# Optimization experiments

Hardware: AMD Instinct MI355X
Metric: run time of the kernel (lower is better)

Reference implementation:

```python
import jax, jax.numpy as jnp
import numpy as np
import math

N_HEAD = 16

def _rope(x):
    # x: [B, H, T, D], D even; interleaved-pair rotation as in the torch code
    B, H, T, D = x.shape
    theta = 10000.0 ** (-2.0 * jnp.arange(D // 2, dtype=x.dtype) / D)  # [D/2]
    pos = jnp.arange(T, dtype=x.dtype)[:, None]                        # [T,1]
    ang = pos * theta[None, :]                                          # [T, D/2]
    sin, cos = jnp.sin(ang), jnp.cos(ang)
    x1, x2 = x[..., ::2], x[..., 1::2]
    x1r = x1 * cos - x2 * sin
    x2r = x1 * sin + x2 * cos
    # re-interleave
    out = jnp.stack([x1r, x2r], axis=-1).reshape(B, H, T, D)
    return out

def setup_inputs() -> dict:
    key = jax.random.key(0)
    ks = jax.random.split(key, 3)
    B, T, C = 4, 2048, 1024
    x = jax.random.normal(ks[0], (B, T, C), dtype=jnp.float32)
    W_qkv = jax.random.normal(ks[1], (C, 3 * C), dtype=jnp.float32) * (1.0 / math.sqrt(C))
    b_qkv = jnp.zeros((3 * C,), dtype=jnp.float32)
    W_proj = jax.random.normal(ks[2], (C, C), dtype=jnp.float32) * (1.0 / math.sqrt(C))
    b_proj = jnp.zeros((C,), dtype=jnp.float32)
    return {"x": x, "W_qkv": W_qkv, "b_qkv": b_qkv, "W_proj": W_proj, "b_proj": b_proj}

def reference(x, W_qkv, b_qkv, W_proj, b_proj):
    B, T, C = x.shape
    H = N_HEAD
    D = C // H
    qkv = x @ W_qkv + b_qkv                      # [B,T,3C]
    q, k, v = jnp.split(qkv, 3, axis=-1)
    def to_heads(t):
        return t.reshape(B, T, H, D).transpose(0, 2, 1, 3)  # [B,H,T,D]
    q, k, v = to_heads(q), to_heads(k), to_heads(v)
    q = _rope(q)
    k = _rope(k)
    att = jnp.einsum('bhqd,bhkd->bhqk', q, k) * (1.0 / math.sqrt(D))
    mask = jnp.tril(jnp.ones((T, T), dtype=bool))
    att = jnp.where(mask[None, None, :, :], att, -jnp.inf)
    att = jax.nn.softmax(att, axis=-1)
    y = jnp.einsum('bhqk,bhkd->bhqd', att, v)    # [B,H,T,D]
    y = y.transpose(0, 2, 1, 3).reshape(B, T, C)
    return y @ W_proj + b_proj
```

## Files before the change

kernel.cpp:

```cpp
#include <hip/hip_runtime.h>
#include <cstddef>

#define B_DIM 4
#define T_DIM 2048
#define C_DIM 1024
#define H_DIM 16
#define D_DIM 64
#define C3_DIM 3072

typedef __attribute__((ext_vector_type(8))) _Float16 f16x8;
typedef __attribute__((ext_vector_type(4))) _Float16 f16x4;
typedef __attribute__((ext_vector_type(4))) float f32x4;

typedef const __attribute__((address_space(1))) unsigned int* gptr_t;
typedef __attribute__((address_space(3))) unsigned int* lptr_t;

#define QSCALE 0.180336850073f
#define NTHETA 0.41524101186f

__global__ __launch_bounds__(256) void prep(
    const float* __restrict__ x, _Float16* __restrict__ xh,
    const float* __restrict__ Wq, _Float16* __restrict__ Wqt,
    const float* __restrict__ Wp, _Float16* __restrict__ Wpt)
{
    __shared__ float tile[64][65];
    const int z = blockIdx.x, tid = threadIdx.x;

    if (z < 8192) {
        size_t i = (size_t)z * 1024 + tid * 4;
        float4 v = *(const float4*)&x[i];
        f16x4 o = { (_Float16)v.x, (_Float16)v.y, (_Float16)v.z, (_Float16)v.w };
        *(f16x4*)&xh[i] = o;
        return;
    }

    const float* W;
    _Float16* Wt;
    int N, idx;
    if (z < 8960) { W = Wq; Wt = Wqt; N = C3_DIM; idx = z - 8192; }
    else          { W = Wp; Wt = Wpt; N = C_DIM;  idx = z - 8960; }
    const int K = C_DIM;
    const int nblk = N / 64;
    const int n0 = (idx % nblk) * 64, k0 = (idx / nblk) * 64;

    const int tx = tid & 15, ty = tid >> 4;
#pragma unroll
    for (int it = 0; it < 4; ++it) {
        int r = it * 16 + ty;
        *(float4*)&tile[r][tx * 4] =
            *(const float4*)&W[(size_t)(k0 + r) * N + n0 + tx * 4];
    }
    __syncthreads();
    int c = tid >> 2, t0 = (tid & 3) * 16;
    __align__(16) _Float16 tmp[16];
#pragma unroll
    for (int j = 0; j < 16; ++j) tmp[j] = (_Float16)tile[t0 + j][c];
    _Float16* o = Wt + (size_t)(n0 + c) * K + k0 + t0;
    *(f16x8*)o = *(f16x8*)&tmp[0];
    *(f16x8*)(o + 8) = *(f16x8*)&tmp[8];
}

#define ISSUE_SLICE(BUF, S, KT)                                               \
    do {                                                                      \
        const _Float16* agk = ag + (KT) * 64 + (S) * 32;                      \
        const _Float16* bgk = bg + (KT) * 64 + (S) * 32;                      \
        __builtin_amdgcn_global_load_lds((gptr_t)(const void*)(agk),          \
            (lptr_t)(void*)&Af[BUF][S][w * 2 + 0][0][0], 16, 0, 0);           \
        __builtin_amdgcn_global_load_lds((gptr_t)(const void*)(agk + 16 * K), \
            (lptr_t)(void*)&Af[BUF][S][w * 2 + 1][0][0], 16, 0, 0);           \
        __builtin_amdgcn_global_load_lds((gptr_t)(const void*)(bgk),          \
            (lptr_t)(void*)&Bf[BUF][S][w][0][0], 16, 0, 0);                   \
    } while (0)

#define COMPUTE_SLICE(BUF, S, SWAPPED)                                        \
    do {                                                                      \
        f16x8 av[4], bv[4];                                                   \
        _Pragma("unroll")                                                     \
        for (int i = 0; i < 4; ++i) {                                         \
            av[i] = *(const f16x8*)&Af[BUF][S][wm * 4 + i][lane][0];          \
            bv[i] = *(const f16x8*)&Bf[BUF][S][wn * 4 + i][lane][0];          \
        }                                                                     \
        __builtin_amdgcn_s_setprio(1);                                        \
        _Pragma("unroll")                                                     \
        for (int i = 0; i < 4; ++i)                                           \
            _Pragma("unroll")                                                 \
            for (int j = 0; j < 4; ++j)                                       \
                acc[i][j] = (SWAPPED)                                         \
                    ? __builtin_amdgcn_mfma_f32_16x16x32_f16(                 \
                          bv[j], av[i], acc[i][j], 0, 0, 0)                   \
                    : __builtin_amdgcn_mfma_f32_16x16x32_f16(                 \
                          av[i], bv[j], acc[i][j], 0, 0, 0);                  \
        __builtin_amdgcn_s_setprio(0);                                        \
    } while (0)

#define KLOOP(SWAPPED)                                                        \
    do {                                                                      \
        const int NT = K / 64;                                                \
        ISSUE_SLICE(0, 0, 0);                                                 \
        ISSUE_SLICE(0, 1, 0);                                                 \
        for (int t = 0; t < NT - 1; ++t) {                                    \
            const int cb = t & 1, nb = cb ^ 1;                                \
            ISSUE_SLICE(nb, 0, t + 1);                                        \
            asm volatile("s_waitcnt vmcnt(6)" ::: "memory");                  \
            __builtin_amdgcn_s_barrier();                                     \
            COMPUTE_SLICE(cb, 0, SWAPPED);                                    \
            ISSUE_SLICE(nb, 1, t + 1);                                        \
            asm volatile("s_waitcnt vmcnt(6)" ::: "memory");                  \
            __builtin_amdgcn_s_barrier();                                     \
            COMPUTE_SLICE(cb, 1, SWAPPED);                                    \
        }                                                                     \
        {                                                                     \
            const int cb = (NT - 1) & 1;                                      \
            asm volatile("s_waitcnt vmcnt(3)" ::: "memory");                  \
            __builtin_amdgcn_s_barrier();                                     \
            COMPUTE_SLICE(cb, 0, SWAPPED);                                    \
            asm volatile("s_waitcnt vmcnt(0)" ::: "memory");                  \
            __builtin_amdgcn_s_barrier();                                     \
            COMPUTE_SLICE(cb, 1, SWAPPED);                                    \
        }                                                                     \
    } while (0)

__global__ __launch_bounds__(512, 2) void gemm_qkv(
    const _Float16* __restrict__ A, const _Float16* __restrict__ Bt,
    const float* __restrict__ bias,
    _Float16* __restrict__ Qb, _Float16* __restrict__ Kb, _Float16* __restrict__ Vt)
{
    __shared__ __align__(16) _Float16 Af[2][2][16][64][8];
    __shared__ __align__(16) _Float16 Bf[2][2][8][64][8];
    const int tid = threadIdx.x;
    const int lane = tid & 63, w = tid >> 6;
    const int lm = lane & 15, lq = lane >> 4;
    const int wm = w >> 1, wn = w & 1;
    const int m0 = blockIdx.y * 256, n0 = blockIdx.x * 128;
    const int K = C_DIM;

    const _Float16* ag = A + (size_t)(m0 + w * 32 + lm) * K + lq * 8;
    const _Float16* bg = Bt + (size_t)(n0 + w * 16 + lm) * K + lq * 8;

    f32x4 acc[4][4];
#pragma unroll
    for (int i = 0; i < 4; ++i)
#pragma unroll
        for (int j = 0; j < 4; ++j) acc[i][j] = (f32x4){0.f, 0.f, 0.f, 0.f};

    const bool is_v = (n0 >= 2 * C_DIM);

    if (!is_v) {
        KLOOP(true);

        const bool is_q = (n0 < C_DIM);
        const float scale = is_q ? QSCALE : 1.0f;
        _Float16* dstbase = is_q ? Qb : Kb;
#pragma unroll
        for (int j = 0; j < 4; ++j) {
            int col = n0 + wn * 64 + j * 16 + lq * 4;
            int d0 = col & 63;
            int h = (col & (C_DIM - 1)) >> 6;
            float4 b4 = *(const float4*)&bias[col];
            float th0 = exp2f(-NTHETA * (float)(d0 >> 1));
            float th1 = exp2f(-NTHETA * (float)((d0 >> 1) + 1));
#pragma unroll
            for (int i = 0; i < 4; ++i) {
                int tg = m0 + wm * 64 + i * 16 + lm;
                int bb = tg >> 11, tl = tg & (T_DIM - 1);
                float v0 = acc[i][j][0] + b4.x;
                float v1 = acc[i][j][1] + b4.y;
                float v2 = acc[i][j][2] + b4.z;
                float v3 = acc[i][j][3] + b4.w;
                float s0, c0, s1, c1;
                __sincosf((float)tl * th0, &s0, &c0);
                __sincosf((float)tl * th1, &s1, &c1);
                f16x4 o = { (_Float16)((v0 * c0 - v1 * s0) * scale),
                            (_Float16)((v0 * s0 + v1 * c0) * scale),
                            (_Float16)((v2 * c1 - v3 * s1) * scale),
                            (_Float16)((v2 * s1 + v3 * c1) * scale) };
                *(f16x4*)&dstbase[((size_t)(bb * 16 + h) * T_DIM + tl) * 64 + d0] = o;
            }
        }
    } else {
        KLOOP(false);

#pragma unroll
        for (int i = 0; i < 4; ++i) {
            int t4 = m0 + wm * 64 + i * 16 + lq * 4;
            int bb = t4 >> 11, tl = t4 & (T_DIM - 1);
#pragma unroll
            for (int j = 0; j < 4; ++j) {
                int col = n0 + wn * 64 + j * 16 + lm;
                int dfull = col - 2 * C_DIM;
                int h = dfull >> 6, d = dfull & 63;
                float bc = bias[col];
                f16x4 o = { (_Float16)(acc[i][j][0] + bc),
                            (_Float16)(acc[i][j][1] + bc),
                            (_Float16)(acc[i][j][2] + bc),
                            (_Float16)(acc[i][j][3] + bc) };
                *(f16x4*)&Vt[((size_t)(bb * 16 + h) * 64 + d) * T_DIM + tl] = o;
            }
        }
    }
}

template <bool OUT_HALF>
__global__ __launch_bounds__(512, 2) void gemm_bt(
    const _Float16* __restrict__ A, const _Float16* __restrict__ Bt,
    const float* __restrict__ bias, void* __restrict__ Cout,
    int M, int N, int K)
{
    __shared__ __align__(16) _Float16 Af[2][2][16][64][8];
    __shared__ __align__(16) _Float16 Bf[2][2][8][64][8];
    const int tid = threadIdx.x;
    const int lane = tid & 63, w = tid >> 6;
    const int lm = lane & 15, lq = lane >> 4;
    const int wm = w >> 1, wn = w & 1;
    const int m0 = blockIdx.y * 256, n0 = blockIdx.x * 128;

    const _Float16* ag = A + (size_t)(m0 + w * 32 + lm) * K + lq * 8;
    const _Float16* bg = Bt + (size_t)(n0 + w * 16 + lm) * K + lq * 8;

    f32x4 acc[4][4];
#pragma unroll
    for (int i = 0; i < 4; ++i)
#pragma unroll
        for (int j = 0; j < 4; ++j) acc[i][j] = (f32x4){0.f, 0.f, 0.f, 0.f};

    KLOOP(true);

#pragma unroll
    for (int i = 0; i < 4; ++i) {
        size_t row = (size_t)(m0 + wm * 64 + i * 16 + lm);
#pragma unroll
        for (int j = 0; j < 4; ++j) {
            int col = n0 + wn * 64 + j * 16 + lq * 4;
            float4 b4 = *(const float4*)&bias[col];
            float v0 = acc[i][j][0] + b4.x;
            float v1 = acc[i][j][1] + b4.y;
            float v2 = acc[i][j][2] + b4.z;
            float v3 = acc[i][j][3] + b4.w;
            if (OUT_HALF) {
                f16x4 o = { (_Float16)v0, (_Float16)v1, (_Float16)v2, (_Float16)v3 };
                *(f16x4*)&((_Float16*)Cout)[row * N + col] = o;
            } else {
                float4 o = make_float4(v0, v1, v2, v3);
                *(float4*)&((float*)Cout)[row * N + col] = o;
            }
        }
    }
}

__global__ __launch_bounds__(256) void attn_mfma(
    const _Float16* __restrict__ Qb, const _Float16* __restrict__ Kb,
    const _Float16* __restrict__ Vt, _Float16* __restrict__ yb)
{
    __shared__ __align__(16) _Float16 Kf[8][64][8];
    __shared__ __align__(16) _Float16 Vf[8][64][8];
    __shared__ __align__(16) _Float16 Pb[4][16][88];

    const int tid = threadIdx.x;
    const int bh = blockIdx.x;
    const int qt = 31 - blockIdx.y;
    const int b = bh >> 4, h = bh & 15;
    const int lane = tid & 63, w = tid >> 6;
    const int m = lane & 15, qq = lane >> 4;

    const _Float16* qrow = Qb +
        ((size_t)bh * T_DIM + qt * 64 + w * 16 + m) * D_DIM + qq * 8;
    f16x8 qreg[2];
    qreg[0] = *(const f16x8*)qrow;
    qreg[1] = *(const f16x8*)(qrow + 32);

    float l_i = 0.f;
    f32x4 acc[4];
#pragma unroll
    for (int db = 0; db < 4; ++db) acc[db] = (f32x4){0.f, 0.f, 0.f, 0.f};

    const _Float16* kg0 = Kb + (size_t)bh * T_DIM * D_DIM +
                          (size_t)(w * 16 + m) * D_DIM + qq * 8;
    const _Float16* vg0 = Vt + (size_t)bh * D_DIM * T_DIM +
                          (size_t)(w * 16 + m) * T_DIM + qq * 8;

    f16x8 kr0 = *(const f16x8*)(kg0);
    f16x8 kr1 = *(const f16x8*)(kg0 + 32);
    f16x8 vr0 = *(const f16x8*)(vg0);
    f16x8 vr1 = *(const f16x8*)(vg0 + 32);

    for (int kt = 0; kt <= qt; ++kt) {
        __syncthreads();
        *(f16x8*)&Kf[w * 2 + 0][lane][0] = kr0;
        *(f16x8*)&Kf[w * 2 + 1][lane][0] = kr1;
        *(f16x8*)&Vf[w * 2 + 0][lane][0] = vr0;
        *(f16x8*)&Vf[w * 2 + 1][lane][0] = vr1;
        __syncthreads();

        int ktn = (kt < qt) ? kt + 1 : kt;
        kr0 = *(const f16x8*)(kg0 + (size_t)ktn * 64 * D_DIM);
        kr1 = *(const f16x8*)(kg0 + (size_t)ktn * 64 * D_DIM + 32);
        vr0 = *(const f16x8*)(vg0 + ktn * 64);
        vr1 = *(const f16x8*)(vg0 + ktn * 64 + 32);

        f32x4 sv[4];
#pragma unroll
        for (int nb = 0; nb < 4; ++nb) {
            f32x4 s = (f32x4){0.f, 0.f, 0.f, 0.f};
            s = __builtin_amdgcn_mfma_f32_16x16x32_f16(
                *(const f16x8*)&Kf[nb * 2 + 0][lane][0], qreg[0], s, 0, 0, 0);
            s = __builtin_amdgcn_mfma_f32_16x16x32_f16(
                *(const f16x8*)&Kf[nb * 2 + 1][lane][0], qreg[1], s, 0, 0, 0);
            sv[nb] = s;
        }

        if (kt == qt) {
            int qlocal = w * 16 + m;
#pragma unroll
            for (int nb = 0; nb < 4; ++nb) {
                int tb = nb * 16 + qq * 4;
#pragma unroll
                for (int r = 0; r < 4; ++r)
                    if (tb + r > qlocal) sv[nb][r] = -1e30f;
            }
        }

        float ll = 0.f;
#pragma unroll
        for (int nb = 0; nb < 4; ++nb) {
            float p0 = exp2f(sv[nb][0]);
            float p1 = exp2f(sv[nb][1]);
            float p2 = exp2f(sv[nb][2]);
            float p3 = exp2f(sv[nb][3]);
            sv[nb][0] = p0; sv[nb][1] = p1; sv[nb][2] = p2; sv[nb][3] = p3;
            ll += (p0 + p1) + (p2 + p3);
        }
        l_i += ll;

#pragma unroll
        for (int nb = 0; nb < 4; ++nb) {
            f16x4 pv = { (_Float16)sv[nb][0], (_Float16)sv[nb][1],
                         (_Float16)sv[nb][2], (_Float16)sv[nb][3] };
            *(f16x4*)&Pb[w][m][nb * 16 + qq * 4] = pv;
        }

        f16x8 pf0 = *(const f16x8*)&Pb[w][m][0 * 32 + qq * 8];
        f16x8 pf1 = *(const f16x8*)&Pb[w][m][1 * 32 + qq * 8];

#pragma unroll
        for (int db = 0; db < 4; ++db) {
            acc[db] = __builtin_amdgcn_mfma_f32_16x16x32_f16(
                *(const f16x8*)&Vf[db * 2 + 0][lane][0], pf0, acc[db], 0, 0, 0);
            acc[db] = __builtin_amdgcn_mfma_f32_16x16x32_f16(
                *(const f16x8*)&Vf[db * 2 + 1][lane][0], pf1, acc[db], 0, 0, 0);
        }
    }

    l_i += __shfl_xor(l_i, 16);
    l_i += __shfl_xor(l_i, 32);

    float inv = 1.0f / l_i;
    _Float16* yrow = yb + (size_t)(b * T_DIM + qt * 64 + w * 16 + m) * C_DIM +
                     h * D_DIM + qq * 4;
#pragma unroll
    for (int db = 0; db < 4; ++db) {
        f16x4 o = { (_Float16)(acc[db][0] * inv), (_Float16)(acc[db][1] * inv),
                    (_Float16)(acc[db][2] * inv), (_Float16)(acc[db][3] * inv) };
        *(f16x4*)(yrow + db * 16) = o;
    }
}

extern "C" void kernel_launch(void* const* d_in, const int* in_sizes, int n_in,
                              void* d_out, int out_size, void* d_ws, size_t ws_size,
                              hipStream_t stream)
{
    const float* x     = (const float*)d_in[0];
    const float* Wqkv  = (const float*)d_in[1];
    const float* bqkv  = (const float*)d_in[2];
    const float* Wproj = (const float*)d_in[3];
    const float* bproj = (const float*)d_in[4];
    float* out = (float*)d_out;

    char* ws = (char*)d_ws;
    _Float16* xh  = (_Float16*)(ws);
    _Float16* yh  = (_Float16*)(ws + 16777216ull);
    _Float16* Qb  = (_Float16*)(ws + 33554432ull);
    _Float16* Kb  = (_Float16*)(ws + 50331648ull);
    _Float16* Vt  = (_Float16*)(ws + 67108864ull);
    _Float16* Wqt = (_Float16*)(ws + 83886080ull);
    _Float16* Wpt = (_Float16*)(ws + 90177536ull);

    prep<<<dim3(9216), dim3(256), 0, stream>>>(x, xh, Wqkv, Wqt, Wproj, Wpt);

    gemm_qkv<<<dim3(C3_DIM / 128, (B_DIM * T_DIM) / 256), dim3(512), 0, stream>>>(
        xh, Wqt, bqkv, Qb, Kb, Vt);

    attn_mfma<<<dim3(B_DIM * H_DIM, T_DIM / 64), dim3(256), 0, stream>>>(
        Qb, Kb, Vt, yh);

    gemm_bt<false><<<dim3(C_DIM / 128, (B_DIM * T_DIM) / 256), dim3(512), 0, stream>>>(
        yh, Wpt, bproj, out, B_DIM * T_DIM, C_DIM, C_DIM);
}
```

Before: 287.0 us.

## Double-buffer attention K/V tiles with direct global-to-LDS async loads

Replaces the register-staged K/V prefetch in the attention kernel with global_load_lds transfers into a double-buffered LDS tile. The next tile's loads are issued before computing on the current one, synchronised with vmcnt waits and raw s_barrier. This removes VGPR staging and the LDS store step, and aims to overlap memory latency with MFMA work. In exchange it doubles K/V LDS use, and correctness relies on hand-written waitcnt values and the LDS address layout that the direct-to-LDS builtin writes.

```diff
diff --git a/kernel.cpp b/kernel.cpp
--- a/kernel.cpp
+++ b/kernel.cpp
@@ -247,12 +247,26 @@
     }
 }
 
+#define ATTN_ISSUE_KV(BUF, KT)                                                \
+    do {                                                                      \
+        const _Float16* kgk = kg0 + (size_t)(KT) * 64 * D_DIM;                \
+        const _Float16* vgk = vg0 + (KT) * 64;                                \
+        __builtin_amdgcn_global_load_lds((gptr_t)(const void*)(kgk),          \
+            (lptr_t)(void*)&Kf[BUF][w * 2 + 0][0][0], 16, 0, 0);              \
+        __builtin_amdgcn_global_load_lds((gptr_t)(const void*)(kgk + 32),     \
+            (lptr_t)(void*)&Kf[BUF][w * 2 + 1][0][0], 16, 0, 0);              \
+        __builtin_amdgcn_global_load_lds((gptr_t)(const void*)(vgk),          \
+            (lptr_t)(void*)&Vf[BUF][w * 2 + 0][0][0], 16, 0, 0);              \
+        __builtin_amdgcn_global_load_lds((gptr_t)(const void*)(vgk + 32),     \
+            (lptr_t)(void*)&Vf[BUF][w * 2 + 1][0][0], 16, 0, 0);              \
+    } while (0)
+
 __global__ __launch_bounds__(256) void attn_mfma(
     const _Float16* __restrict__ Qb, const _Float16* __restrict__ Kb,
     const _Float16* __restrict__ Vt, _Float16* __restrict__ yb)
 {
-    __shared__ __align__(16) _Float16 Kf[8][64][8];
-    __shared__ __align__(16) _Float16 Vf[8][64][8];
+    __shared__ __align__(16) _Float16 Kf[2][8][64][8];
+    __shared__ __align__(16) _Float16 Vf[2][8][64][8];
     __shared__ __align__(16) _Float16 Pb[4][16][88];
 
     const int tid = threadIdx.x;
@@ -278,33 +292,26 @@
     const _Float16* vg0 = Vt + (size_t)bh * D_DIM * T_DIM +
                           (size_t)(w * 16 + m) * T_DIM + qq * 8;
 
-    f16x8 kr0 = *(const f16x8*)(kg0);
-    f16x8 kr1 = *(const f16x8*)(kg0 + 32);
-    f16x8 vr0 = *(const f16x8*)(vg0);
-    f16x8 vr1 = *(const f16x8*)(vg0 + 32);
+    ATTN_ISSUE_KV(0, 0);
+    int cur = 0;
 
     for (int kt = 0; kt <= qt; ++kt) {
-        __syncthreads();
-        *(f16x8*)&Kf[w * 2 + 0][lane][0] = kr0;
-        *(f16x8*)&Kf[w * 2 + 1][lane][0] = kr1;
-        *(f16x8*)&Vf[w * 2 + 0][lane][0] = vr0;
-        *(f16x8*)&Vf[w * 2 + 1][lane][0] = vr1;
-        __syncthreads();
-
-        int ktn = (kt < qt) ? kt + 1 : kt;
-        kr0 = *(const f16x8*)(kg0 + (size_t)ktn * 64 * D_DIM);
-        kr1 = *(const f16x8*)(kg0 + (size_t)ktn * 64 * D_DIM + 32);
-        vr0 = *(const f16x8*)(vg0 + ktn * 64);
-        vr1 = *(const f16x8*)(vg0 + ktn * 64 + 32);
+        if (kt < qt) {
+            ATTN_ISSUE_KV(cur ^ 1, kt + 1);
+            asm volatile("s_waitcnt vmcnt(4)" ::: "memory");
+        } else {
+            asm volatile("s_waitcnt vmcnt(0)" ::: "memory");
+        }
+        __builtin_amdgcn_s_barrier();
 
         f32x4 sv[4];
 #pragma unroll
         for (int nb = 0; nb < 4; ++nb) {
             f32x4 s = (f32x4){0.f, 0.f, 0.f, 0.f};
             s = __builtin_amdgcn_mfma_f32_16x16x32_f16(
-                *(const f16x8*)&Kf[nb * 2 + 0][lane][0], qreg[0], s, 0, 0, 0);
+                *(const f16x8*)&Kf[cur][nb * 2 + 0][lane][0], qreg[0], s, 0, 0, 0);
             s = __builtin_amdgcn_mfma_f32_16x16x32_f16(
-                *(const f16x8*)&Kf[nb * 2 + 1][lane][0], qreg[1], s, 0, 0, 0);
+                *(const f16x8*)&Kf[cur][nb * 2 + 1][lane][0], qreg[1], s, 0, 0, 0);
             sv[nb] = s;
         }
 
@@ -344,10 +351,13 @@
 #pragma unroll
         for (int db = 0; db < 4; ++db) {
             acc[db] = __builtin_amdgcn_mfma_f32_16x16x32_f16(
-                *(const f16x8*)&Vf[db * 2 + 0][lane][0], pf0, acc[db], 0, 0, 0);
+                *(const f16x8*)&Vf[cur][db * 2 + 0][lane][0], pf0, acc[db], 0, 0, 0);
             acc[db] = __builtin_amdgcn_mfma_f32_16x16x32_f16(
-                *(const f16x8*)&Vf[db * 2 + 1][lane][0], pf1, acc[db], 0, 0, 0);
-        }
+                *(const f16x8*)&Vf[cur][db * 2 + 1][lane][0], pf1, acc[db], 0, 0, 0);
+        }
+
+        __builtin_amdgcn_s_barrier();
+        cur ^= 1;
     }
 
     l_i += __shfl_xor(l_i, 16);
```

New measurement: 293.7 us. +2.3%, slower.
